# Optimization experiments

Measured on AMD Instinct MI355X. Metric: run time of the kernel, lower is better.

Reference implementation:

```python
import jax, jax.numpy as jnp
import numpy as np
from jax import lax

H = 384
W = 384
N = H * W                 # flattened pixel count
N_LOC = N // 2            # unknown pixels with 3x3 matting-Laplacian stencils
KCM = 20                  # color-mixture KNN size
K_IU = 5                  # intra-unknown KNN size
NNZ_CM = N_LOC * KCM


def setup_inputs() -> dict:
    key = jax.random.key(0)
    ks = jax.random.split(key, 16)
    f32 = jnp.float32
    i32 = jnp.int32
    inp = {}
    inp["CM_weights"] = jax.random.uniform(ks[0], (N,), f32)
    inp["LOC_weights"] = jax.random.uniform(ks[1], (N,), f32)
    inp["IU_weights"] = jax.random.uniform(ks[2], (N,), f32)
    inp["KU_weights"] = jax.random.uniform(ks[3], (N,), f32)
    inp["lmbda"] = jnp.full((1,), 100.0, f32)
    inp["kToUconf"] = jax.random.uniform(ks[4], (N,), f32)
    inp["known"] = jax.random.uniform(ks[5], (N,), f32)
    inp["kToU"] = jax.random.uniform(ks[6], (N,), f32)
    inp["Wcm_data"] = jax.random.uniform(ks[7], (NNZ_CM,), f32)
    inp["LOC_flows"] = jax.random.uniform(ks[8], (9, 9, N_LOC), f32)
    inp["IU_flows"] = jax.random.uniform(ks[9], (N_LOC, K_IU), f32)
    inp["Wcm_row"] = jax.random.randint(ks[10], (NNZ_CM,), 0, N, dtype=i32)
    inp["Wcm_col"] = jax.random.randint(ks[11], (NNZ_CM,), 0, N, dtype=i32)
    # interior pixels so all 9 stencil neighbours are valid
    inp["LOC_inInd"] = jax.random.randint(ks[12], (N_LOC,), W + 1, N - W - 1, dtype=i32)
    inp["IU_inInd"] = jax.random.randint(ks[13], (N_LOC,), 0, N, dtype=i32)
    inp["IU_neighInd"] = jax.random.randint(ks[14], (N_LOC, K_IU), 0, N, dtype=i32)
    inp["width"] = W
    inp["cg_steps"] = 30
    return inp


def reference(CM_weights, LOC_weights, IU_weights, KU_weights, lmbda,
              kToUconf, known, kToU, Wcm_data, LOC_flows, IU_flows,
              Wcm_row, Wcm_col, LOC_inInd, IU_inInd, IU_neighInd,
              width, cg_steps):
    n = kToU.shape[0]
    seg = lambda v, i: jax.ops.segment_sum(v, i, num_segments=n)

    # --- color mixture: Wcm scaled by diag(CM_weights); L = diag(rowsum) - Wcm; Lcm = L^T L
    cm_vals = CM_weights[Wcm_row] * Wcm_data
    rs_cm = seg(cm_vals, Wcm_row)

    # --- matting Laplacian: 9x9 flows per unknown pixel over 3x3 stencil
    offs = jnp.array([-1 - width, -1, -1 + width, -width, 0, width,
                      1 - width, 1, 1 + width], dtype=LOC_inInd.dtype)
    neigh = LOC_inInd[:, None] + offs[None, :]                    # [n_loc, 9]
    fl = LOC_flows * LOC_weights[LOC_inInd][None, None, :]        # [9, 9, n_loc]
    nloc = neigh.shape[0]
    # entry (row=neigh[k,i], col=neigh[k,j]) has value fl[j, i, k]
    vals_m = jnp.transpose(fl, (2, 1, 0)).reshape(-1)
    rows_m = jnp.broadcast_to(neigh[:, :, None], (nloc, 9, 9)).reshape(-1)
    cols_m = jnp.broadcast_to(neigh[:, None, :], (nloc, 9, 9)).reshape(-1)
    rows_ms = jnp.concatenate([rows_m, cols_m])
    cols_ms = jnp.concatenate([cols_m, rows_m])
    vals_ms = 0.5 * jnp.concatenate([vals_m, vals_m])             # W = 0.5 (W + W^T)
    rs_m = seg(vals_ms, rows_ms)

    # --- intra-unknowns KNN affinities
    fiu = IU_flows * IU_weights[IU_inInd][:, None]                # [n_iu, K]
    rows_c0 = jnp.broadcast_to(IU_inInd[:, None], IU_neighInd.shape).reshape(-1)
    cols_c0 = IU_neighInd.reshape(-1)
    rows_cs = jnp.concatenate([rows_c0, cols_c0])
    cols_cs = jnp.concatenate([cols_c0, rows_c0])
    vals_cs = 0.5 * jnp.concatenate([fiu.reshape(-1), fiu.reshape(-1)])
    rs_c = seg(vals_cs, rows_cs)

    # --- diagonal data terms: KU + lmbda*known
    diag_ku = KU_weights * kToUconf + lmbda[0] * known
    b = diag_ku * kToU

    def matvec(v):
        # Lcm @ v = L^T (L v), keeping L in factored COO form
        Lv = rs_cm * v - seg(cm_vals * v[Wcm_col], Wcm_row)
        lcm = rs_cm * Lv - seg(cm_vals * Lv[Wcm_row], Wcm_col)
        lm = rs_m * v - seg(vals_ms * v[cols_ms], rows_ms)
        lc = rs_c * v - seg(vals_cs * v[cols_cs], rows_cs)
        return lcm + lm + lc + diag_ku * v

    def cg_step(carry, _):
        x, r, p, rs = carry
        Ap = matvec(p)
        alpha = rs / jnp.vdot(p, Ap)
        x = x + alpha * p
        r = r - alpha * Ap
        rs_new = jnp.vdot(r, r)
        p = r + (rs_new / rs) * p
        return (x, r, p, rs_new), None

    x0 = jnp.zeros_like(b)  # x0 = 0 as in MattingSolver
    (x, _, _, _), _ = lax.scan(cg_step, (x0, b, b, jnp.vdot(b, b)), None, length=cg_steps)
    return x
```

## Files before the change

### kernel.cpp

```cpp
#include <hip/hip_runtime.h>


#define TPB 256

__device__ __forceinline__ float blockReduce256(float v) {
  #pragma unroll
  for (int o = 32; o > 0; o >>= 1) v += __shfl_down(v, o, 64);
  __shared__ float s[4];
  int lane = threadIdx.x & 63, wv = threadIdx.x >> 6;
  if (lane == 0) s[wv] = v;
  __syncthreads();
  return (threadIdx.x == 0) ? (s[0] + s[1] + s[2] + s[3]) : 0.f;
}

__global__ void k_init0(const float* __restrict__ KUw, const float* __restrict__ kToUconf,
                        const float* __restrict__ lmbda, const float* __restrict__ known,
                        const float* __restrict__ kToU,
                        float* __restrict__ diag_ku, float* __restrict__ r,
                        float* __restrict__ p, float* __restrict__ x,
                        int* __restrict__ CNT, float* __restrict__ scal, int N)
{
  int i = blockIdx.x * TPB + threadIdx.x;
  if (i < 80) scal[i] = 0.f;
  if (i < 3 * N) CNT[i] = 0;
  float red = 0.f;
  if (i < N) {
    float dk = KUw[i] * kToUconf[i] + lmbda[0] * known[i];
    diag_ku[i] = dk;
    float b = dk * kToU[i];
    r[i] = b; p[i] = b; x[i] = 0.f;
    red = b * b;
  }
  float v = blockReduce256(red);
  if (threadIdx.x == 0) atomicAdd(&scal[0], v);
}

__global__ void k_prep(float* __restrict__ LOC_flows, const int* __restrict__ LOC_inInd,
                       const float* __restrict__ LOCw, int NLOC)
{
  int k = blockIdx.x * TPB + threadIdx.x;
  float Fl[81];
  #pragma unroll
  for (int m = 0; m < 81; ++m) Fl[m] = LOC_flows[(size_t)m * NLOC + k];
  float hw = 0.5f * LOCw[LOC_inInd[k]];
  int idx = 0;
  #pragma unroll
  for (int a = 0; a < 9; ++a)
    #pragma unroll
    for (int b = a + 1; b < 9; ++b) {
      LOC_flows[(size_t)idx * NLOC + k] = hw * (Fl[a * 9 + b] + Fl[b * 9 + a]);
      ++idx;
    }
}

__global__ void k_hist(const int* __restrict__ Wrow, const int* __restrict__ Wcol,
                       const int* __restrict__ LOC_inInd, const int* __restrict__ width_p,
                       const int* __restrict__ IU_inInd, const int* __restrict__ IU_neighInd,
                       int* __restrict__ CNT,
                       unsigned short* __restrict__ tr, unsigned short* __restrict__ tc,
                       unsigned short* __restrict__ tU,
                       int NLOC, int N, int B0, int B1)
{
  int blk = blockIdx.x;
  if (blk < B0) {
    int e = blk * TPB + threadIdx.x;
    tr[e] = (unsigned short)atomicAdd(&CNT[Wrow[e]], 1);
    tc[e] = (unsigned short)atomicAdd(&CNT[N + Wcol[e]], 1);
  } else if (blk < B1) {
    int k = (blk - B0) * TPB + threadIdx.x;
    int wd = *width_p;
    int base = LOC_inInd[k];
    const int offs[9] = {-1 - wd, -1, -1 + wd, -wd, 0, wd, 1 - wd, 1, 1 + wd};
    #pragma unroll
    for (int a = 0; a < 9; ++a)
      tU[a * NLOC + k] = (unsigned short)atomicAdd(&CNT[2 * N + base + offs[a]], 1);
  } else {
    int k = (blk - B1) * TPB + threadIdx.x;
    tU[14 * NLOC + k] = (unsigned short)atomicAdd(&CNT[2 * N + IU_inInd[k]], 1);
    #pragma unroll
    for (int j = 0; j < 5; ++j)
      tU[(9 + j) * NLOC + k] =
          (unsigned short)atomicAdd(&CNT[2 * N + IU_neighInd[k * 5 + j]], 1);
  }
}

__global__ void k_scan1(int* __restrict__ OFF, int* __restrict__ bsum, int tot)
{
  __shared__ int s[TPB];
  int gid = blockIdx.x * TPB + threadIdx.x;
  int v = (gid < tot) ? OFF[gid] : 0;
  s[threadIdx.x] = v;
  __syncthreads();
  #pragma unroll
  for (int o = 1; o < TPB; o <<= 1) {
    int t = (threadIdx.x >= o) ? s[threadIdx.x - o] : 0;
    __syncthreads();
    s[threadIdx.x] += t;
    __syncthreads();
  }
  if (gid < tot) OFF[gid] = s[threadIdx.x] - v;
  if (threadIdx.x == TPB - 1) bsum[blockIdx.x] = s[threadIdx.x];
}

__global__ void k_scan2(int* __restrict__ bsum, int nPerArr)
{
  __shared__ int s[1024];
  int base = blockIdx.x * nPerArr;
  int v = (threadIdx.x < nPerArr) ? bsum[base + threadIdx.x] : 0;
  s[threadIdx.x] = v;
  __syncthreads();
  for (int o = 1; o < 1024; o <<= 1) {
    int t = (threadIdx.x >= o) ? s[threadIdx.x - o] : 0;
    __syncthreads();
    s[threadIdx.x] += t;
    __syncthreads();
  }
  if (threadIdx.x < nPerArr) bsum[base + threadIdx.x] = s[threadIdx.x] - v;
}

__global__ void k_scan3(int* __restrict__ OFF, const int* __restrict__ bsum, int tot)
{
  int gid = blockIdx.x * TPB + threadIdx.x;
  if (gid < tot) OFF[gid] += bsum[blockIdx.x];
}

__global__ void k_fill(const float* __restrict__ CMw, const float* __restrict__ Wcm_data,
                       const int* __restrict__ Wrow, const int* __restrict__ Wcol,
                       const int* __restrict__ LOC_inInd, const int* __restrict__ width_p,
                       const int* __restrict__ IU_inInd, const int* __restrict__ IU_neighInd,
                       const int* __restrict__ OFF,
                       const unsigned short* __restrict__ tr, const unsigned short* __restrict__ tc,
                       const unsigned short* __restrict__ tU,
                       int2* __restrict__ csrPk, int2* __restrict__ cscPk,
                       int* __restrict__ gU,
                       int NLOC, int N, int B0, int B1)
{
  int blk = blockIdx.x;
  if (blk < B0) {
    int e = blk * TPB + threadIdx.x;
    int row = Wrow[e], col = Wcol[e];
    int cv = __float_as_int(CMw[row] * Wcm_data[e]);
    csrPk[OFF[row] + tr[e]] = make_int2(col, cv);
    cscPk[OFF[N + col] + tc[e]] = make_int2(row, cv);
  } else if (blk < B1) {
    int k = (blk - B0) * TPB + threadIdx.x;
    int wd = *width_p;
    int base = LOC_inInd[k];
    const int offs[9] = {-1 - wd, -1, -1 + wd, -wd, 0, wd, 1 - wd, 1, 1 + wd};
    #pragma unroll
    for (int a = 0; a < 9; ++a)
      gU[OFF[2 * N + base + offs[a]] + tU[a * NLOC + k]] = a * NLOC + k;
  } else {
    int k = (blk - B1) * TPB + threadIdx.x;
    gU[OFF[2 * N + IU_inInd[k]] + tU[14 * NLOC + k]] = 14 * NLOC + k;
    #pragma unroll
    for (int j = 0; j < 5; ++j)
      gU[OFF[2 * N + IU_neighInd[k * 5 + j]] + tU[(9 + j) * NLOC + k]] =
          (9 + j) * NLOC + k;
  }
}

__global__ void k_it1(const float* __restrict__ p,
                      const float* __restrict__ S2, const int* __restrict__ LOC_inInd,
                      const int* __restrict__ width_p,
                      const float* __restrict__ IU_flows, const int* __restrict__ IU_inInd,
                      const int* __restrict__ IU_neighInd, const float* __restrict__ IUw,
                      const float* __restrict__ diag_ku,
                      const int* __restrict__ OFF, const int2* __restrict__ csrPk,
                      float* __restrict__ u_all,
                      float* __restrict__ Lv, float* __restrict__ rs_cm,
                      float* __restrict__ pAp_t,
                      int NNZ, int NLOC, int N, int B0, int B1)
{
  int blk = blockIdx.x;
  float red = 0.f;
  if (blk < B0) {
    int k = blk * TPB + threadIdx.x;
    int wd = *width_p;
    int base = LOC_inInd[k];
    const int offs[9] = {-1 - wd, -1, -1 + wd, -wd, 0, wd, 1 - wd, 1, 1 + wd};
    float pv[9];
    #pragma unroll
    for (int a = 0; a < 9; ++a) pv[a] = p[base + offs[a]];
    float u[9] = {0.f, 0.f, 0.f, 0.f, 0.f, 0.f, 0.f, 0.f, 0.f};
    float qf = 0.f;
    int idx = 0;
    #pragma unroll
    for (int a = 0; a < 9; ++a)
      #pragma unroll
      for (int b = a + 1; b < 9; ++b) {
        float sv = S2[(size_t)idx * NLOC + k];
        ++idx;
        float d = pv[a] - pv[b];
        float t = sv * d;
        u[a] += t; u[b] -= t;
        qf += t * d;
      }
    #pragma unroll
    for (int a = 0; a < 9; ++a) u_all[a * NLOC + k] = u[a];
    red = qf;
  } else if (blk < B1) {
    int k = (blk - B0) * TPB + threadIdx.x;
    int r0 = IU_inInd[k];
    float hw = 0.5f * IUw[r0];
    float pr = p[r0];
    int c[5]; float w[5];
    #pragma unroll
    for (int j = 0; j < 5; ++j) {
      c[j] = IU_neighInd[k * 5 + j];
      w[j] = hw * IU_flows[k * 5 + j];
    }
    float pc[5];
    #pragma unroll
    for (int j = 0; j < 5; ++j) pc[j] = p[c[j]];
    float qf = 0.f, asum = 0.f;
    #pragma unroll
    for (int j = 0; j < 5; ++j) {
      float d = pr - pc[j];
      float uA = w[j] * d;
      u_all[(9 + j) * NLOC + k] = -uA;
      asum += uA;
      qf += uA * d;
    }
    u_all[14 * NLOC + k] = asum;
    red = qf;
  } else {
    int i = (blk - B1) * TPB + threadIdx.x;
    float pi = p[i];
    int s = OFF[i];
    int e = (i == N - 1) ? NNZ : OFF[i + 1];
    float acc = 0.f, rs = 0.f;
    int q = s;
    for (; q + 8 <= e; q += 8) {
      int2 ed[8];
      #pragma unroll
      for (int m = 0; m < 8; ++m) ed[m] = csrPk[q + m];
      float g[8];
      #pragma unroll
      for (int m = 0; m < 8; ++m) g[m] = p[ed[m].x];
      #pragma unroll
      for (int m = 0; m < 8; ++m) {
        float cv = __int_as_float(ed[m].y);
        rs += cv;
        acc += cv * (pi - g[m]);
      }
    }
    for (; q + 4 <= e; q += 4) {
      int2 ed[4];
      #pragma unroll
      for (int m = 0; m < 4; ++m) ed[m] = csrPk[q + m];
      float g[4];
      #pragma unroll
      for (int m = 0; m < 4; ++m) g[m] = p[ed[m].x];
      #pragma unroll
      for (int m = 0; m < 4; ++m) {
        float cv = __int_as_float(ed[m].y);
        rs += cv;
        acc += cv * (pi - g[m]);
      }
    }
    for (; q < e; ++q) {
      int2 ed = csrPk[q];
      float cv = __int_as_float(ed.y);
      rs += cv;
      acc += cv * (pi - p[ed.x]);
    }
    Lv[i] = acc;
    rs_cm[i] = rs;
    red = diag_ku[i] * pi * pi + acc * acc;
  }
  float v = blockReduce256(red);
  if (threadIdx.x == 0) atomicAdd(pAp_t, v);
}

__global__ void k_it2(float* __restrict__ x, float* __restrict__ r,
                      const float* __restrict__ p, const float* __restrict__ Lv,
                      const float* __restrict__ rs_cm, const float* __restrict__ diag_ku,
                      const int* __restrict__ OFF,
                      const int2* __restrict__ cscPk,
                      const int* __restrict__ gU, const float* __restrict__ u_all,
                      const float* __restrict__ rs_t, const float* __restrict__ pAp_t,
                      float* __restrict__ rs_t1,
                      int NNZ, int NLOC, int N)
{
  int i = blockIdx.x * TPB + threadIdx.x;
  float alpha = rs_t[0] / pAp_t[0];
  float tg = 0.f;
  {
    int s0 = OFF[2 * N + i];
    int e0 = (i == N - 1) ? 15 * NLOC : OFF[2 * N + i + 1];
    int q = s0;
    for (; q + 8 <= e0; q += 8) {
      int g[8];
      #pragma unroll
      for (int m = 0; m < 8; ++m) g[m] = gU[q + m];
      float u[8];
      #pragma unroll
      for (int m = 0; m < 8; ++m) u[m] = u_all[g[m]];
      #pragma unroll
      for (int m = 0; m < 8; ++m) tg += u[m];
    }
    for (; q + 4 <= e0; q += 4) {
      int g[4];
      #pragma unroll
      for (int m = 0; m < 4; ++m) g[m] = gU[q + m];
      float u[4];
      #pragma unroll
      for (int m = 0; m < 4; ++m) u[m] = u_all[g[m]];
      #pragma unroll
      for (int m = 0; m < 4; ++m) tg += u[m];
    }
    for (; q < e0; ++q) tg += u_all[gU[q]];
  }
  float sc = 0.f;
  {
    int s0 = OFF[N + i];
    int e0 = (i == N - 1) ? NNZ : OFF[N + i + 1];
    int q = s0;
    for (; q + 8 <= e0; q += 8) {
      int2 ed[8];
      #pragma unroll
      for (int m = 0; m < 8; ++m) ed[m] = cscPk[q + m];
      float l[8];
      #pragma unroll
      for (int m = 0; m < 8; ++m) l[m] = Lv[ed[m].x];
      #pragma unroll
      for (int m = 0; m < 8; ++m) sc += __int_as_float(ed[m].y) * l[m];
    }
    for (; q + 4 <= e0; q += 4) {
      int2 ed[4];
      #pragma unroll
      for (int m = 0; m < 4; ++m) ed[m] = cscPk[q + m];
      float l[4];
      #pragma unroll
      for (int m = 0; m < 4; ++m) l[m] = Lv[ed[m].x];
      #pragma unroll
      for (int m = 0; m < 4; ++m) sc += __int_as_float(ed[m].y) * l[m];
    }
    for (; q < e0; ++q) {
      int2 ed = cscPk[q];
      sc += __int_as_float(ed.y) * Lv[ed.x];
    }
  }
  float pi = p[i];
  float Ap = diag_ku[i] * pi + rs_cm[i] * Lv[i] - sc + tg;
  x[i] += alpha * pi;
  float rn = r[i] - alpha * Ap;
  r[i] = rn;
  float v = blockReduce256(rn * rn);
  if (threadIdx.x == 0) atomicAdd(rs_t1, v);
}

__global__ void k_it3(float* __restrict__ p, const float* __restrict__ r,
                      const float* __restrict__ rs_new, const float* __restrict__ rs_old, int N)
{
  int i = blockIdx.x * TPB + threadIdx.x;
  float beta = rs_new[0] / rs_old[0];
  p[i] = r[i] + beta * p[i];
}

extern "C" void kernel_launch(void* const* d_in, const int* in_sizes, int n_in,
                              void* d_out, int out_size, void* d_ws, size_t ws_size,
                              hipStream_t stream)
{
  const float* CMw       = (const float*)d_in[0];
  const float* LOCw      = (const float*)d_in[1];
  const float* IUw       = (const float*)d_in[2];
  const float* KUw       = (const float*)d_in[3];
  const float* lmbda     = (const float*)d_in[4];
  const float* kToUconf  = (const float*)d_in[5];
  const float* known     = (const float*)d_in[6];
  const float* kToU      = (const float*)d_in[7];
  const float* Wcm_data  = (const float*)d_in[8];
  float*       LOC_flows = (float*)d_in[9];
  const float* IU_flows  = (const float*)d_in[10];
  const int*   Wrow      = (const int*)d_in[11];
  const int*   Wcol      = (const int*)d_in[12];
  const int*   LOC_inInd = (const int*)d_in[13];
  const int*   IU_inInd  = (const int*)d_in[14];
  const int*   IU_neighInd = (const int*)d_in[15];
  const int*   width_p   = (const int*)d_in[16];
  const int CG_STEPS = 30;

  const int N    = in_sizes[0];
  const int NNZ  = in_sizes[8];
  const int NLOC = in_sizes[13];

  float* x       = (float*)d_out;
  float* r       = (float*)d_ws;
  float* p       = r + N;
  float* Lv      = p + N;
  float* rs_cm   = Lv + N;
  float* diag_ku = rs_cm + N;
  int2*  csrPk   = (int2*)(diag_ku + N);
  int2*  cscPk   = csrPk + (size_t)NNZ;
  int*   gU      = (int*)(cscPk + (size_t)NNZ);
  int*   OFF     = gU + (size_t)15 * NLOC;
  unsigned short* tr = (unsigned short*)(OFF + (size_t)3 * N);
  unsigned short* tc = tr + (size_t)NNZ;
  unsigned short* tU = tc + (size_t)NNZ;
  float* u_all   = (float*)tr;
  int*   bsum    = (int*)(tU + (size_t)15 * NLOC);
  float* scal    = (float*)(bsum + 3 * (N / TPB));

  const int Bn = N / TPB;
  const int Bz = NNZ / TPB;
  const int Bl = NLOC / TPB;
  const int Z3 = 3 * Bn;

  k_init0<<<Z3, TPB, 0, stream>>>(KUw, kToUconf, lmbda, known, kToU,
                                  diag_ku, r, p, x, OFF, scal, N);
  k_prep<<<Bl, TPB, 0, stream>>>(LOC_flows, LOC_inInd, LOCw, NLOC);
  k_hist<<<Bz + 2 * Bl, TPB, 0, stream>>>(Wrow, Wcol, LOC_inInd, width_p,
                                          IU_inInd, IU_neighInd, OFF,
                                          tr, tc, tU, NLOC, N, Bz, Bz + Bl);
  k_scan1<<<Z3, TPB, 0, stream>>>(OFF, bsum, 3 * N);
  k_scan2<<<3, 1024, 0, stream>>>(bsum, Bn);
  k_scan3<<<Z3, TPB, 0, stream>>>(OFF, bsum, 3 * N);
  k_fill<<<Bz + 2 * Bl, TPB, 0, stream>>>(CMw, Wcm_data, Wrow, Wcol,
                                          LOC_inInd, width_p, IU_inInd, IU_neighInd,
                                          OFF, tr, tc, tU,
                                          csrPk, cscPk, gU,
                                          NLOC, N, Bz, Bz + Bl);

  for (int t = 0; t < CG_STEPS; ++t) {
    k_it1<<<2 * Bl + Bn, TPB, 0, stream>>>(
        p, LOC_flows, LOC_inInd, width_p,
        IU_flows, IU_inInd, IU_neighInd, IUw,
        diag_ku, OFF, csrPk, u_all, Lv, rs_cm, scal + 40 + t,
        NNZ, NLOC, N, Bl, 2 * Bl);
    k_it2<<<Bn, TPB, 0, stream>>>(
        x, r, p, Lv, rs_cm, diag_ku, OFF, cscPk, gU, u_all,
        scal + t, scal + 40 + t, scal + t + 1, NNZ, NLOC, N);
    if (t + 1 < CG_STEPS)
      k_it3<<<Bn, TPB, 0, stream>>>(p, r, scal + t + 1, scal + t, N);
  }
}
```

Baseline: 1.879 ms.

## Scatter contributions into destination-sorted order so gather kernel reads contiguously

Instead of building a CSC copy of the color-mixture matrix and a gather index list for stencil contributions, the fill phase now stores, for each source entry, its slot in destination-sorted order. During each CG iteration the producer kernel scatters per-entry products (cv*Lv and stencil u values) directly to those slots, so the consumer kernel only sums contiguous runs, with no indirect index loads or random Lv gathers. This trades random reads in k_it2 for random writes in k_it1, and adds an extra pass over the CSR row to emit NNZ scattered writes per iteration.

```diff
diff --git a/kernel.cpp b/kernel.cpp
--- a/kernel.cpp
+++ b/kernel.cpp
@@ -131,8 +131,8 @@
                        const int* __restrict__ OFF,
                        const unsigned short* __restrict__ tr, const unsigned short* __restrict__ tc,
                        const unsigned short* __restrict__ tU,
-                       int2* __restrict__ csrPk, int2* __restrict__ cscPk,
-                       int* __restrict__ gU,
+                       int2* __restrict__ csrPk, int* __restrict__ cscPos,
+                       int* __restrict__ gInv,
                        int NLOC, int N, int B0, int B1)
 {
   int blk = blockIdx.x;
@@ -140,8 +140,9 @@
     int e = blk * TPB + threadIdx.x;
     int row = Wrow[e], col = Wcol[e];
     int cv = __float_as_int(CMw[row] * Wcm_data[e]);
-    csrPk[OFF[row] + tr[e]] = make_int2(col, cv);
-    cscPk[OFF[N + col] + tc[e]] = make_int2(row, cv);
+    int cs = OFF[row] + tr[e];
+    csrPk[cs] = make_int2(col, cv);
+    cscPos[cs] = OFF[N + col] + tc[e];
   } else if (blk < B1) {
     int k = (blk - B0) * TPB + threadIdx.x;
     int wd = *width_p;
@@ -149,14 +150,14 @@
     const int offs[9] = {-1 - wd, -1, -1 + wd, -wd, 0, wd, 1 - wd, 1, 1 + wd};
     #pragma unroll
     for (int a = 0; a < 9; ++a)
-      gU[OFF[2 * N + base + offs[a]] + tU[a * NLOC + k]] = a * NLOC + k;
+      gInv[a * NLOC + k] = OFF[2 * N + base + offs[a]] + tU[a * NLOC + k];
   } else {
     int k = (blk - B1) * TPB + threadIdx.x;
-    gU[OFF[2 * N + IU_inInd[k]] + tU[14 * NLOC + k]] = 14 * NLOC + k;
+    gInv[14 * NLOC + k] = OFF[2 * N + IU_inInd[k]] + tU[14 * NLOC + k];
     #pragma unroll
     for (int j = 0; j < 5; ++j)
-      gU[OFF[2 * N + IU_neighInd[k * 5 + j]] + tU[(9 + j) * NLOC + k]] =
-          (9 + j) * NLOC + k;
+      gInv[(9 + j) * NLOC + k] =
+          OFF[2 * N + IU_neighInd[k * 5 + j]] + tU[(9 + j) * NLOC + k];
   }
 }
 
@@ -167,7 +168,8 @@
                       const int* __restrict__ IU_neighInd, const float* __restrict__ IUw,
                       const float* __restrict__ diag_ku,
                       const int* __restrict__ OFF, const int2* __restrict__ csrPk,
-                      float* __restrict__ u_all,
+                      const int* __restrict__ cscPos, const int* __restrict__ gInv,
+                      float* __restrict__ u_sorted, float* __restrict__ LvS,
                       float* __restrict__ Lv, float* __restrict__ rs_cm,
                       float* __restrict__ pAp_t,
                       int NNZ, int NLOC, int N, int B0, int B1)
@@ -179,6 +181,9 @@
     int wd = *width_p;
     int base = LOC_inInd[k];
     const int offs[9] = {-1 - wd, -1, -1 + wd, -wd, 0, wd, 1 - wd, 1, 1 + wd};
+    int gi[9];
+    #pragma unroll
+    for (int a = 0; a < 9; ++a) gi[a] = gInv[a * NLOC + k];
     float pv[9];
     #pragma unroll
     for (int a = 0; a < 9; ++a) pv[a] = p[base + offs[a]];
@@ -197,13 +202,17 @@
         qf += t * d;
       }
     #pragma unroll
-    for (int a = 0; a < 9; ++a) u_all[a * NLOC + k] = u[a];
+    for (int a = 0; a < 9; ++a) u_sorted[gi[a]] = u[a];
     red = qf;
   } else if (blk < B1) {
     int k = (blk - B0) * TPB + threadIdx.x;
     int r0 = IU_inInd[k];
     float hw = 0.5f * IUw[r0];
     float pr = p[r0];
+    int gi[6];
+    #pragma unroll
+    for (int j = 0; j < 5; ++j) gi[j] = gInv[(9 + j) * NLOC + k];
+    gi[5] = gInv[14 * NLOC + k];
     int c[5]; float w[5];
     #pragma unroll
     for (int j = 0; j < 5; ++j) {
@@ -218,11 +227,11 @@
     for (int j = 0; j < 5; ++j) {
       float d = pr - pc[j];
       float uA = w[j] * d;
-      u_all[(9 + j) * NLOC + k] = -uA;
+      u_sorted[gi[j]] = -uA;
       asum += uA;
       qf += uA * d;
     }
-    u_all[14 * NLOC + k] = asum;
+    u_sorted[gi[5]] = asum;
     red = qf;
   } else {
     int i = (blk - B1) * TPB + threadIdx.x;
@@ -267,6 +276,17 @@
     }
     Lv[i] = acc;
     rs_cm[i] = rs;
+    q = s;
+    for (; q + 4 <= e; q += 4) {
+      int2 e0 = csrPk[q], e1 = csrPk[q + 1], e2 = csrPk[q + 2], e3 = csrPk[q + 3];
+      int c0 = cscPos[q], c1 = cscPos[q + 1], c2 = cscPos[q + 2], c3 = cscPos[q + 3];
+      LvS[c0] = __int_as_float(e0.y) * acc;
+      LvS[c1] = __int_as_float(e1.y) * acc;
+      LvS[c2] = __int_as_float(e2.y) * acc;
+      LvS[c3] = __int_as_float(e3.y) * acc;
+    }
+    for (; q < e; ++q)
+      LvS[cscPos[q]] = __int_as_float(csrPk[q].y) * acc;
     red = diag_ku[i] * pi * pi + acc * acc;
   }
   float v = blockReduce256(red);
@@ -277,8 +297,7 @@
                       const float* __restrict__ p, const float* __restrict__ Lv,
                       const float* __restrict__ rs_cm, const float* __restrict__ diag_ku,
                       const int* __restrict__ OFF,
-                      const int2* __restrict__ cscPk,
-                      const int* __restrict__ gU, const float* __restrict__ u_all,
+                      const float* __restrict__ LvS, const float* __restrict__ u_sorted,
                       const float* __restrict__ rs_t, const float* __restrict__ pAp_t,
                       float* __restrict__ rs_t1,
                       int NNZ, int NLOC, int N)
@@ -287,60 +306,43 @@
   float alpha = rs_t[0] / pAp_t[0];
   float tg = 0.f;
   {
-    int s0 = OFF[2 * N + i];
+    int q = OFF[2 * N + i];
     int e0 = (i == N - 1) ? 15 * NLOC : OFF[2 * N + i + 1];
-    int q = s0;
     for (; q + 8 <= e0; q += 8) {
-      int g[8];
-      #pragma unroll
-      for (int m = 0; m < 8; ++m) g[m] = gU[q + m];
       float u[8];
       #pragma unroll
-      for (int m = 0; m < 8; ++m) u[m] = u_all[g[m]];
+      for (int m = 0; m < 8; ++m) u[m] = u_sorted[q + m];
       #pragma unroll
       for (int m = 0; m < 8; ++m) tg += u[m];
     }
     for (; q + 4 <= e0; q += 4) {
-      int g[4];
-      #pragma unroll
-      for (int m = 0; m < 4; ++m) g[m] = gU[q + m];
       float u[4];
       #pragma unroll
-      for (int m = 0; m < 4; ++m) u[m] = u_all[g[m]];
+      for (int m = 0; m < 4; ++m) u[m] = u_sorted[q + m];
       #pragma unroll
       for (int m = 0; m < 4; ++m) tg += u[m];
     }
-    for (; q < e0; ++q) tg += u_all[gU[q]];
+    for (; q < e0; ++q) tg += u_sorted[q];
   }
   float sc = 0.f;
   {
-    int s0 = OFF[N + i];
+    int q = OFF[N + i];
     int e0 = (i == N - 1) ? NNZ : OFF[N + i + 1];
-    int q = s0;
     for (; q + 8 <= e0; q += 8) {
-      int2 ed[8];
-      #pragma unroll
-      for (int m = 0; m < 8; ++m) ed[m] = cscPk[q + m];
       float l[8];
       #pragma unroll
-      for (int m = 0; m < 8; ++m) l[m] = Lv[ed[m].x];
-      #pragma unroll
-      for (int m = 0; m < 8; ++m) sc += __int_as_float(ed[m].y) * l[m];
+      for (int m = 0; m < 8; ++m) l[m] = LvS[q + m];
+      #pragma unroll
+      for (int m = 0; m < 8; ++m) sc += l[m];
     }
     for (; q + 4 <= e0; q += 4) {
-      int2 ed[4];
-      #pragma unroll
-      for (int m = 0; m < 4; ++m) ed[m] = cscPk[q + m];
       float l[4];
       #pragma unroll
-      for (int m = 0; m < 4; ++m) l[m] = Lv[ed[m].x];
-      #pragma unroll
-      for (int m = 0; m < 4; ++m) sc += __int_as_float(ed[m].y) * l[m];
-    }
-    for (; q < e0; ++q) {
-      int2 ed = cscPk[q];
-      sc += __int_as_float(ed.y) * Lv[ed.x];
-    }
+      for (int m = 0; m < 4; ++m) l[m] = LvS[q + m];
+      #pragma unroll
+      for (int m = 0; m < 4; ++m) sc += l[m];
+    }
+    for (; q < e0; ++q) sc += LvS[q];
   }
   float pi = p[i];
   float Ap = diag_ku[i] * pi + rs_cm[i] * Lv[i] - sc + tg;
@@ -393,13 +395,14 @@
   float* rs_cm   = Lv + N;
   float* diag_ku = rs_cm + N;
   int2*  csrPk   = (int2*)(diag_ku + N);
-  int2*  cscPk   = csrPk + (size_t)NNZ;
-  int*   gU      = (int*)(cscPk + (size_t)NNZ);
-  int*   OFF     = gU + (size_t)15 * NLOC;
+  int*   cscPos  = (int*)(csrPk + (size_t)NNZ);
+  float* LvS     = (float*)(cscPos + (size_t)NNZ);
+  int*   gInv    = (int*)(LvS + (size_t)NNZ);
+  int*   OFF     = gInv + (size_t)15 * NLOC;
   unsigned short* tr = (unsigned short*)(OFF + (size_t)3 * N);
   unsigned short* tc = tr + (size_t)NNZ;
   unsigned short* tU = tc + (size_t)NNZ;
-  float* u_all   = (float*)tr;
+  float* u_sorted = (float*)tr;
   int*   bsum    = (int*)(tU + (size_t)15 * NLOC);
   float* scal    = (float*)(bsum + 3 * (N / TPB));
 
@@ -420,17 +423,18 @@
   k_fill<<<Bz + 2 * Bl, TPB, 0, stream>>>(CMw, Wcm_data, Wrow, Wcol,
                                           LOC_inInd, width_p, IU_inInd, IU_neighInd,
                                           OFF, tr, tc, tU,
-                                          csrPk, cscPk, gU,
+                                          csrPk, cscPos, gInv,
                                           NLOC, N, Bz, Bz + Bl);
 
   for (int t = 0; t < CG_STEPS; ++t) {
     k_it1<<<2 * Bl + Bn, TPB, 0, stream>>>(
         p, LOC_flows, LOC_inInd, width_p,
         IU_flows, IU_inInd, IU_neighInd, IUw,
-        diag_ku, OFF, csrPk, u_all, Lv, rs_cm, scal + 40 + t,
+        diag_ku, OFF, csrPk, cscPos, gInv,
+        u_sorted, LvS, Lv, rs_cm, scal + 40 + t,
         NNZ, NLOC, N, Bl, 2 * Bl);
     k_it2<<<Bn, TPB, 0, stream>>>(
-        x, r, p, Lv, rs_cm, diag_ku, OFF, cscPk, gU, u_all,
+        x, r, p, Lv, rs_cm, diag_ku, OFF, LvS, u_sorted,
         scal + t, scal + 40 + t, scal + t + 1, NNZ, NLOC, N);
     if (t + 1 < CG_STEPS)
       k_it3<<<Bn, TPB, 0, stream>>>(p, r, scal + t + 1, scal + t, N);
```

New measurement: 2.222 ms. +18.2%, slower.

## Fuse CG direction update into matvec by storing p and r interleaved

Applied to the files above, without the earlier changes.

Removes the separate p = r + beta*p kernel. p_old and r are stored together as a float2 array, and every consumer rebuilds the current p on the fly with an fma using beta. This saves one launch and one full-vector pass per CG iteration. In exchange, every gather in the matvec now loads 8 bytes instead of 4 and does an extra fma, which raises the scattered-read traffic in the SpMV.

```diff
diff --git a/kernel.cpp b/kernel.cpp
--- a/kernel.cpp
+++ b/kernel.cpp
@@ -16,8 +16,8 @@
 __global__ void k_init0(const float* __restrict__ KUw, const float* __restrict__ kToUconf,
                         const float* __restrict__ lmbda, const float* __restrict__ known,
                         const float* __restrict__ kToU,
-                        float* __restrict__ diag_ku, float* __restrict__ r,
-                        float* __restrict__ p, float* __restrict__ x,
+                        float* __restrict__ diag_ku, float2* __restrict__ PR,
+                        float* __restrict__ x,
                         int* __restrict__ CNT, float* __restrict__ scal, int N)
 {
   int i = blockIdx.x * TPB + threadIdx.x;
@@ -28,7 +28,8 @@
     float dk = KUw[i] * kToUconf[i] + lmbda[0] * known[i];
     diag_ku[i] = dk;
     float b = dk * kToU[i];
-    r[i] = b; p[i] = b; x[i] = 0.f;
+    PR[i] = make_float2(b, b);
+    x[i] = 0.f;
     red = b * b;
   }
   float v = blockReduce256(red);
@@ -160,7 +161,7 @@
   }
 }
 
-__global__ void k_it1(const float* __restrict__ p,
+__global__ void k_it1(const float2* __restrict__ PR,
                       const float* __restrict__ S2, const int* __restrict__ LOC_inInd,
                       const int* __restrict__ width_p,
                       const float* __restrict__ IU_flows, const int* __restrict__ IU_inInd,
@@ -169,10 +170,12 @@
                       const int* __restrict__ OFF, const int2* __restrict__ csrPk,
                       float* __restrict__ u_all,
                       float* __restrict__ Lv, float* __restrict__ rs_cm,
+                      const float* __restrict__ rsN, const float* __restrict__ rsO, int first,
                       float* __restrict__ pAp_t,
                       int NNZ, int NLOC, int N, int B0, int B1)
 {
   int blk = blockIdx.x;
+  float beta = first ? 0.f : rsN[0] / rsO[0];
   float red = 0.f;
   if (blk < B0) {
     int k = blk * TPB + threadIdx.x;
@@ -181,7 +184,10 @@
     const int offs[9] = {-1 - wd, -1, -1 + wd, -wd, 0, wd, 1 - wd, 1, 1 + wd};
     float pv[9];
     #pragma unroll
-    for (int a = 0; a < 9; ++a) pv[a] = p[base + offs[a]];
+    for (int a = 0; a < 9; ++a) {
+      float2 pr = PR[base + offs[a]];
+      pv[a] = __builtin_fmaf(beta, pr.x, pr.y);
+    }
     float u[9] = {0.f, 0.f, 0.f, 0.f, 0.f, 0.f, 0.f, 0.f, 0.f};
     float qf = 0.f;
     int idx = 0;
@@ -203,7 +209,8 @@
     int k = (blk - B0) * TPB + threadIdx.x;
     int r0 = IU_inInd[k];
     float hw = 0.5f * IUw[r0];
-    float pr = p[r0];
+    float2 prr = PR[r0];
+    float pr = __builtin_fmaf(beta, prr.x, prr.y);
     int c[5]; float w[5];
     #pragma unroll
     for (int j = 0; j < 5; ++j) {
@@ -212,7 +219,10 @@
     }
     float pc[5];
     #pragma unroll
-    for (int j = 0; j < 5; ++j) pc[j] = p[c[j]];
+    for (int j = 0; j < 5; ++j) {
+      float2 pp = PR[c[j]];
+      pc[j] = __builtin_fmaf(beta, pp.x, pp.y);
+    }
     float qf = 0.f, asum = 0.f;
     #pragma unroll
     for (int j = 0; j < 5; ++j) {
@@ -226,7 +236,8 @@
     red = qf;
   } else {
     int i = (blk - B1) * TPB + threadIdx.x;
-    float pi = p[i];
+    float2 pri = PR[i];
+    float pi = __builtin_fmaf(beta, pri.x, pri.y);
     int s = OFF[i];
     int e = (i == N - 1) ? NNZ : OFF[i + 1];
     float acc = 0.f, rs = 0.f;
@@ -237,7 +248,10 @@
       for (int m = 0; m < 8; ++m) ed[m] = csrPk[q + m];
       float g[8];
       #pragma unroll
-      for (int m = 0; m < 8; ++m) g[m] = p[ed[m].x];
+      for (int m = 0; m < 8; ++m) {
+        float2 pp = PR[ed[m].x];
+        g[m] = __builtin_fmaf(beta, pp.x, pp.y);
+      }
       #pragma unroll
       for (int m = 0; m < 8; ++m) {
         float cv = __int_as_float(ed[m].y);
@@ -251,7 +265,10 @@
       for (int m = 0; m < 4; ++m) ed[m] = csrPk[q + m];
       float g[4];
       #pragma unroll
-      for (int m = 0; m < 4; ++m) g[m] = p[ed[m].x];
+      for (int m = 0; m < 4; ++m) {
+        float2 pp = PR[ed[m].x];
+        g[m] = __builtin_fmaf(beta, pp.x, pp.y);
+      }
       #pragma unroll
       for (int m = 0; m < 4; ++m) {
         float cv = __int_as_float(ed[m].y);
@@ -262,8 +279,9 @@
     for (; q < e; ++q) {
       int2 ed = csrPk[q];
       float cv = __int_as_float(ed.y);
+      float2 pp = PR[ed.x];
       rs += cv;
-      acc += cv * (pi - p[ed.x]);
+      acc += cv * (pi - __builtin_fmaf(beta, pp.x, pp.y));
     }
     Lv[i] = acc;
     rs_cm[i] = rs;
@@ -273,18 +291,20 @@
   if (threadIdx.x == 0) atomicAdd(pAp_t, v);
 }
 
-__global__ void k_it2(float* __restrict__ x, float* __restrict__ r,
-                      const float* __restrict__ p, const float* __restrict__ Lv,
+__global__ void k_it2(float* __restrict__ x, float2* __restrict__ PR,
+                      const float* __restrict__ Lv,
                       const float* __restrict__ rs_cm, const float* __restrict__ diag_ku,
                       const int* __restrict__ OFF,
                       const int2* __restrict__ cscPk,
                       const int* __restrict__ gU, const float* __restrict__ u_all,
                       const float* __restrict__ rs_t, const float* __restrict__ pAp_t,
+                      const float* __restrict__ rsO, int first,
                       float* __restrict__ rs_t1,
                       int NNZ, int NLOC, int N)
 {
   int i = blockIdx.x * TPB + threadIdx.x;
   float alpha = rs_t[0] / pAp_t[0];
+  float beta = first ? 0.f : rs_t[0] / rsO[0];
   float tg = 0.f;
   {
     int s0 = OFF[2 * N + i];
@@ -342,21 +362,14 @@
       sc += __int_as_float(ed.y) * Lv[ed.x];
     }
   }
-  float pi = p[i];
+  float2 pri = PR[i];
+  float pi = __builtin_fmaf(beta, pri.x, pri.y);
   float Ap = diag_ku[i] * pi + rs_cm[i] * Lv[i] - sc + tg;
   x[i] += alpha * pi;
-  float rn = r[i] - alpha * Ap;
-  r[i] = rn;
+  float rn = pri.y - alpha * Ap;
+  PR[i] = make_float2(pi, rn);
   float v = blockReduce256(rn * rn);
   if (threadIdx.x == 0) atomicAdd(rs_t1, v);
-}
-
-__global__ void k_it3(float* __restrict__ p, const float* __restrict__ r,
-                      const float* __restrict__ rs_new, const float* __restrict__ rs_old, int N)
-{
-  int i = blockIdx.x * TPB + threadIdx.x;
-  float beta = rs_new[0] / rs_old[0];
-  p[i] = r[i] + beta * p[i];
 }
 
 extern "C" void kernel_launch(void* const* d_in, const int* in_sizes, int n_in,
@@ -387,9 +400,8 @@
   const int NLOC = in_sizes[13];
 
   float* x       = (float*)d_out;
-  float* r       = (float*)d_ws;
-  float* p       = r + N;
-  float* Lv      = p + N;
+  float2* PR     = (float2*)d_ws;
+  float* Lv      = (float*)(PR + (size_t)N);
   float* rs_cm   = Lv + N;
   float* diag_ku = rs_cm + N;
   int2*  csrPk   = (int2*)(diag_ku + N);
@@ -409,7 +421,7 @@
   const int Z3 = 3 * Bn;
 
   k_init0<<<Z3, TPB, 0, stream>>>(KUw, kToUconf, lmbda, known, kToU,
-                                  diag_ku, r, p, x, OFF, scal, N);
+                                  diag_ku, PR, x, OFF, scal, N);
   k_prep<<<Bl, TPB, 0, stream>>>(LOC_flows, LOC_inInd, LOCw, NLOC);
   k_hist<<<Bz + 2 * Bl, TPB, 0, stream>>>(Wrow, Wcol, LOC_inInd, width_p,
                                           IU_inInd, IU_neighInd, OFF,
@@ -424,15 +436,17 @@
                                           NLOC, N, Bz, Bz + Bl);
 
   for (int t = 0; t < CG_STEPS; ++t) {
+    const float* rsN = scal + t;
+    const float* rsO = scal + (t == 0 ? 0 : t - 1);
     k_it1<<<2 * Bl + Bn, TPB, 0, stream>>>(
-        p, LOC_flows, LOC_inInd, width_p,
+        PR, LOC_flows, LOC_inInd, width_p,
         IU_flows, IU_inInd, IU_neighInd, IUw,
-        diag_ku, OFF, csrPk, u_all, Lv, rs_cm, scal + 40 + t,
+        diag_ku, OFF, csrPk, u_all, Lv, rs_cm,
+        rsN, rsO, (t == 0) ? 1 : 0, scal + 40 + t,
         NNZ, NLOC, N, Bl, 2 * Bl);
     k_it2<<<Bn, TPB, 0, stream>>>(
-        x, r, p, Lv, rs_cm, diag_ku, OFF, cscPk, gU, u_all,
-        scal + t, scal + 40 + t, scal + t + 1, NNZ, NLOC, N);
-    if (t + 1 < CG_STEPS)
-      k_it3<<<Bn, TPB, 0, stream>>>(p, r, scal + t + 1, scal + t, N);
-  }
-}
+        x, PR, Lv, rs_cm, diag_ku, OFF, cscPk, gU, u_all,
+        rsN, scal + 40 + t, rsO, (t == 0) ? 1 : 0, scal + t + 1,
+        NNZ, NLOC, N);
+  }
+}
```

Result: faster. 1.812 ms (-3.6%).
